# Optimization experiments

Measured on AMD Instinct MI355X. Metric: run time of the kernel, lower is better.

Reference implementation:

```python
import jax, jax.numpy as jnp
import numpy as np

B, N = 4096, 8
C_IMG = 1024          # 256 fpn channels * 4 layers
NODE_CH = 2048        # 8 node concepts * 256
EDGE_CH = 3           # len(edge_concepts) - 1 (HigherPri handled separately)
ACT_CH = 4            # number of unary action predicates
E = N * (N - 1)       # 56 directed edges, fully connected minus self-loops
BBOX_MAX = 1024.0

_idx = np.array([[i, j] for i in range(N) for j in range(N) if i != j], dtype=np.int32)
SRC = jnp.asarray(_idx[:, 0])  # edge_idxs row 0 (message source in PyG NNConv)
DST = jnp.asarray(_idx[:, 1])  # edge_idxs row 1 (aggregation target)


def _lin(key, fin, fout):
    kw, kb = jax.random.split(key)
    s = 1.0 / np.sqrt(fin)
    return (jax.random.uniform(kw, (fin, fout), jnp.float32, -s, s),
            jax.random.uniform(kb, (fout,), jnp.float32, -s, s))


def setup_inputs() -> dict:
    key = jax.random.key(0)
    ks = jax.random.split(key, 16)
    inp = {
        'roi_features': jax.random.normal(ks[0], (B, N, C_IMG), jnp.float32),
        'batch_bboxes': jax.random.uniform(ks[1], (B, N, 4), jnp.float32) * BBOX_MAX,
        'batch_directions': jax.random.normal(ks[2], (B, N, 4), jnp.float32),
        'batch_priorities': jax.random.uniform(ks[3], (B, N), jnp.float32),
    }
    inp['ncp_w1'], inp['ncp_b1'] = _lin(ks[4], C_IMG, 512)
    inp['ncp_w2'], inp['ncp_b2'] = _lin(ks[5], 512, 256)
    inp['ncp_w3'], inp['ncp_b3'] = _lin(ks[6], 256, NODE_CH)
    inp['ep_w1'], inp['ep_b1'] = _lin(ks[7], 8, 256)
    inp['ep_w2'], inp['ep_b2'] = _lin(ks[8], 256, 64)
    inp['ep_w3'], inp['ep_b3'] = _lin(ks[9], 64, (N - 1) * EDGE_CH)
    inp['pr_w1'], inp['pr_b1'] = _lin(ks[10], EDGE_CH + 1, 128)
    inp['pr_w2'], inp['pr_b2'] = _lin(ks[11], 128, NODE_CH * ACT_CH)
    s = 1.0 / np.sqrt(NODE_CH)
    inp['root'] = jax.random.uniform(ks[12], (NODE_CH, ACT_CH), jnp.float32, -s, s)
    inp['bias'] = jnp.zeros((ACT_CH,), jnp.float32)
    return inp


def reference(roi_features, batch_bboxes, batch_directions, batch_priorities,
              ncp_w1, ncp_b1, ncp_w2, ncp_b2, ncp_w3, ncp_b3,
              ep_w1, ep_b1, ep_w2, ep_b2, ep_w3, ep_b3,
              pr_w1, pr_b1, pr_w2, pr_b2, root, bias):
    # node concept predictor: 3-layer MLP + sigmoid over [B, N, C_IMG]
    h = jax.nn.relu(roi_features @ ncp_w1 + ncp_b1)
    h = jax.nn.relu(h @ ncp_w2 + ncp_b2)
    node_concepts = jax.nn.sigmoid(h @ ncp_w3 + ncp_b3)           # [B, N, NODE_CH]

    # edge predictor from bbox (normalized) + direction attributes
    node_attr = jnp.concatenate([batch_bboxes / BBOX_MAX, batch_directions], axis=-1)  # [B,N,8]
    g = jax.nn.relu(node_attr @ ep_w1 + ep_b1)
    g = jax.nn.relu(g @ ep_w2 + ep_b2)
    edge_attr = jax.nn.sigmoid(g @ ep_w3 + ep_b3).reshape(B, N * (N - 1), EDGE_CH)

    # HigherPri channel; original slices pri_mask[:, :, :N-1] (slice [:, :, N:] is empty)
    pri_mask = (batch_priorities[:, :, None] > batch_priorities[:, None, :]).astype(jnp.float32)
    higher_pri = pri_mask[:, :, :N - 1].reshape(B, -1)            # [B, E]
    edge_attr = jnp.concatenate([edge_attr, higher_pri[..., None]], axis=-1)  # [B,E,4]

    # NNConv on batch element 0 only (as in the original forward)
    x = node_concepts[0]                                          # [N, NODE_CH]
    e = edge_attr[0]                                              # [E, EDGE_CH+1]
    w = jax.nn.relu(e @ pr_w1 + pr_b1) @ pr_w2 + pr_b2            # [E, NODE_CH*ACT_CH]
    w = w.reshape(E, NODE_CH, ACT_CH)
    msg = jnp.einsum('ec,eco->eo', x[SRC], w)                     # [E, ACT_CH]
    agg = jax.ops.segment_sum(msg, DST, num_segments=N)           # [N, ACT_CH]
    return agg + x @ root + bias
```

## Files before the change

kernel.cpp:

```cpp
#include <hip/hip_runtime.h>
#include <math.h>

#define CIMG  1024
#define H1F   512
#define H2F   256
#define NODE  2048

#define OFF_H1P  0
#define OFF_H2P  65536
#define OFF_XP   98304
#define OFF_Y2P  163840
#define OFF_EW   172032

__global__ __launch_bounds__(256) void k1_l1_edge(
    const float* __restrict__ roi, const float* __restrict__ w1,
    const float* __restrict__ bbox, const float* __restrict__ dir,
    const float* __restrict__ pri,
    const float* __restrict__ ew1, const float* __restrict__ eb1,
    const float* __restrict__ ew2, const float* __restrict__ eb2,
    const float* __restrict__ ew3, const float* __restrict__ eb3,
    const float* __restrict__ pw1, const float* __restrict__ pb1,
    float* __restrict__ h1part, float* __restrict__ ew_out)
{
    __shared__ float smem[2912];
    const int tid = threadIdx.x;
    const int b = blockIdx.x;

    if (b < 32) {
        float* xin = smem;
        const int kbeg = (b >> 1) * 64;
        const int cbase = (b & 1) * 256;
        for (int idx = tid; idx < 512; idx += 256) {
            int r = idx >> 6, kk = idx & 63;
            xin[idx] = roi[r * CIMG + kbeg + kk];
        }
        __syncthreads();
        const int c = cbase + tid;
        float acc[8] = {0, 0, 0, 0, 0, 0, 0, 0};
        const float* Wp = w1 + (size_t)kbeg * H1F + c;
#pragma unroll 4
        for (int kk = 0; kk < 64; ++kk) {
            float w = Wp[(size_t)kk * H1F];
#pragma unroll
            for (int r = 0; r < 8; ++r) acc[r] += xin[r * 64 + kk] * w;
        }
        float* outp = h1part + (b >> 1) * 4096;
#pragma unroll
        for (int r = 0; r < 8; ++r) outp[r * H1F + c] = acc[r];
        return;
    }

    float* attr = smem;
    float* g1   = smem + 64;
    float* g2   = smem + 2112;
    float* ebuf = smem + 2624;

    if (tid < 64) {
        int r = tid >> 3, j = tid & 7;
        attr[r * 8 + j] = (j < 4) ? bbox[r * 4 + j] * (1.0f / 1024.0f)
                                  : dir[r * 4 + (j - 4)];
    }
    __syncthreads();

    {
        int cc = tid;
        for (int r = 0; r < 8; ++r) {
            float s = eb1[cc];
#pragma unroll
            for (int j = 0; j < 8; ++j) s += attr[r * 8 + j] * ew1[j * 256 + cc];
            g1[r * 256 + cc] = s > 0.f ? s : 0.f;
        }
    }
    __syncthreads();

    for (int idx = tid; idx < 512; idx += 256) {
        int r = idx >> 6, cc = idx & 63;
        float s = eb2[cc];
        for (int j = 0; j < 256; ++j) s += g1[r * 256 + j] * ew2[j * 64 + cc];
        g2[idx] = s > 0.f ? s : 0.f;
    }
    __syncthreads();

    if (tid < 168) {
        int r = tid / 21, q = tid % 21;
        float s = eb3[q];
        for (int j = 0; j < 64; ++j) s += g2[r * 64 + j] * ew3[j * 21 + q];
        ebuf[(tid / 3) * 4 + (tid % 3)] = 1.f / (1.f + expf(-s));
    }
    if (tid < 56) {
        ebuf[tid * 4 + 3] = (pri[tid / 7] > pri[tid % 7]) ? 1.f : 0.f;
    }
    __syncthreads();

    for (int idx = tid; idx < 56 * 128; idx += 256) {
        int e = idx >> 7, t = idx & 127;
        float s = pb1[t];
#pragma unroll
        for (int ch = 0; ch < 4; ++ch) s += ebuf[e * 4 + ch] * pw1[ch * 128 + t];
        ew_out[idx] = s > 0.f ? s : 0.f;
    }
}

__global__ __launch_bounds__(256) void k2_l2(
    const float* __restrict__ h1part, const float* __restrict__ b1,
    const float* __restrict__ w2, float* __restrict__ h2part)
{
    __shared__ float xin[8 * 32];
    const int tid = threadIdx.x;
    const int kbeg = blockIdx.x * 32;

    if (tid < 256) {
        int r = tid >> 5, kk = tid & 31;
        int k = kbeg + kk;
        float v = b1[k];
#pragma unroll
        for (int p = 0; p < 16; ++p) v += h1part[p * 4096 + r * H1F + k];
        xin[r * 32 + kk] = v > 0.f ? v : 0.f;
    }
    __syncthreads();

    const int c = tid;
    float acc[8] = {0, 0, 0, 0, 0, 0, 0, 0};
    const float* Wp = w2 + (size_t)kbeg * H2F + c;
#pragma unroll 4
    for (int kk = 0; kk < 32; ++kk) {
        float w = Wp[(size_t)kk * H2F];
#pragma unroll
        for (int r = 0; r < 8; ++r) acc[r] += xin[r * 32 + kk] * w;
    }
    float* outp = h2part + blockIdx.x * 2048;
#pragma unroll
    for (int r = 0; r < 8; ++r) outp[r * H2F + c] = acc[r];
}

__global__ __launch_bounds__(256) void k3_l3(
    const float* __restrict__ h2part, const float* __restrict__ b2,
    const float* __restrict__ w3, float* __restrict__ xpart)
{
    __shared__ float xin[8 * 64];
    const int tid = threadIdx.x;
    const int kc = blockIdx.x >> 3;
    const int cbase = (blockIdx.x & 7) * 256;
    const int kbeg = kc * 64;

    for (int idx = tid; idx < 512; idx += 256) {
        int r = idx >> 6, kk = idx & 63;
        int k = kbeg + kk;
        float v = b2[k];
#pragma unroll
        for (int p = 0; p < 16; ++p) v += h2part[p * 2048 + r * H2F + k];
        xin[idx] = v > 0.f ? v : 0.f;
    }
    __syncthreads();

    const int c = cbase + tid;
    float acc[8] = {0, 0, 0, 0, 0, 0, 0, 0};
    const float* Wp = w3 + (size_t)kbeg * NODE + c;
#pragma unroll 4
    for (int kk = 0; kk < 64; ++kk) {
        float w = Wp[(size_t)kk * NODE];
#pragma unroll
        for (int r = 0; r < 8; ++r) acc[r] += xin[r * 64 + kk] * w;
    }
    float* outp = xpart + kc * 16384;
#pragma unroll
    for (int r = 0; r < 8; ++r) outp[r * NODE + c] = acc[r];
}

__global__ __launch_bounds__(256) void k4_y2(
    const float* __restrict__ xpart, const float* __restrict__ b3,
    const float* __restrict__ pw2, float* __restrict__ y2part)
{
    const int t = blockIdx.x;
    const int half = blockIdx.y;
    __shared__ float shx[8 * 1024];
    __shared__ float redbuf[4 * 32];
    const int tid = threadIdx.x;

    for (int i = tid; i < 8192; i += 256) {
        int r = i >> 10, cl = i & 1023;
        int c = half * 1024 + cl;
        float v = b3[c];
#pragma unroll
        for (int p = 0; p < 4; ++p) v += xpart[p * 16384 + r * NODE + c];
        shx[i] = 1.f / (1.f + expf(-v));
    }
    __syncthreads();

    float part[8] = {0, 0, 0, 0, 0, 0, 0, 0};
    const float* row = pw2 + (size_t)t * 8192 + half * 4096;
#pragma unroll 4
    for (int it = 0; it < 16; ++it) {
        int j = tid + it * 256;
        float w = row[j];
        int cl = j >> 2;
#pragma unroll
        for (int s = 0; s < 8; ++s) part[s] += shx[s * 1024 + cl] * w;
    }

    const int lane = tid & 63, wave = tid >> 6;
#pragma unroll
    for (int s = 0; s < 8; ++s) {
        part[s] += __shfl_xor(part[s], 4);
        part[s] += __shfl_xor(part[s], 8);
        part[s] += __shfl_xor(part[s], 16);
        part[s] += __shfl_xor(part[s], 32);
    }
    if (lane < 4) {
#pragma unroll
        for (int s = 0; s < 8; ++s) redbuf[wave * 32 + s * 4 + lane] = part[s];
    }
    __syncthreads();
    if (tid < 32) {
        float v = redbuf[tid] + redbuf[32 + tid] + redbuf[64 + tid] + redbuf[96 + tid];
        int s = tid >> 2, o = tid & 3;
        y2part[half * 4096 + (s * 128 + t) * 4 + o] = v;
    }
}

__global__ __launch_bounds__(1024) void k5_final(
    const float* __restrict__ xpart, const float* __restrict__ b3,
    const float* __restrict__ pb2, const float* __restrict__ root,
    const float* __restrict__ bias, const float* __restrict__ ew,
    const float* __restrict__ y2part, float* __restrict__ out)
{
    __shared__ float sdotb[8][2][4], sxr[8][2][4], sagg[8][4];
    const int tid = threadIdx.x;
    const int lane = tid & 63, wave = tid >> 6;

    if (tid < 32) sagg[tid >> 2][tid & 3] = 0.f;
    __syncthreads();

    {
        const int s = wave >> 1, half = wave & 1;
        float pd[4] = {0, 0, 0, 0}, pr[4] = {0, 0, 0, 0};
#pragma unroll 4
        for (int k = 0; k < 16; ++k) {
            int c = half * 1024 + k * 64 + lane;
            float v = b3[c];
#pragma unroll
            for (int p = 0; p < 4; ++p) v += xpart[p * 16384 + s * NODE + c];
            float xv = 1.f / (1.f + expf(-v));
            float4 bv = ((const float4*)pb2)[c];
            float4 rv = ((const float4*)root)[c];
            pd[0] += xv * bv.x; pd[1] += xv * bv.y;
            pd[2] += xv * bv.z; pd[3] += xv * bv.w;
            pr[0] += xv * rv.x; pr[1] += xv * rv.y;
            pr[2] += xv * rv.z; pr[3] += xv * rv.w;
        }
#pragma unroll
        for (int o = 0; o < 4; ++o) {
            for (int off = 32; off; off >>= 1) {
                pd[o] += __shfl_xor(pd[o], off);
                pr[o] += __shfl_xor(pr[o], off);
            }
        }
        if (lane == 0) {
#pragma unroll
            for (int o = 0; o < 4; ++o) {
                sdotb[s][half][o] = pd[o];
                sxr[s][half][o] = pr[o];
            }
        }
    }

    const float* y2a = y2part;
    const float* y2b = y2part + 4096;
    for (int e = wave; e < 56; e += 16) {
        int i = e / 7, jj = e % 7;
        int dst = jj + (jj >= i ? 1 : 0);
        int src = i;
        float pm[4] = {0, 0, 0, 0};
#pragma unroll
        for (int half = 0; half < 2; ++half) {
            int t = lane + half * 64;
            float w = ew[e * 128 + t];
            float4 ya = ((const float4*)y2a)[src * 128 + t];
            float4 yb = ((const float4*)y2b)[src * 128 + t];
            pm[0] += w * (ya.x + yb.x); pm[1] += w * (ya.y + yb.y);
            pm[2] += w * (ya.z + yb.z); pm[3] += w * (ya.w + yb.w);
        }
#pragma unroll
        for (int o = 0; o < 4; ++o)
            for (int off = 32; off; off >>= 1) pm[o] += __shfl_xor(pm[o], off);
        if (lane == 0) {
#pragma unroll
            for (int o = 0; o < 4; ++o) atomicAdd(&sagg[dst][o], pm[o]);
        }
    }
    __syncthreads();

    if (tid < 32) {
        int n = tid >> 2, o = tid & 3;
        float totd = 0.f;
#pragma unroll
        for (int s = 0; s < 8; ++s) totd += sdotb[s][0][o] + sdotb[s][1][o];
        float dn = sdotb[n][0][o] + sdotb[n][1][o];
        float xr = sxr[n][0][o] + sxr[n][1][o];
        out[tid] = sagg[n][o] + (totd - dn) + xr + bias[o];
    }
}

extern "C" void kernel_launch(void* const* d_in, const int* in_sizes, int n_in,
                              void* d_out, int out_size, void* d_ws, size_t ws_size,
                              hipStream_t stream)
{
    (void)in_sizes; (void)n_in; (void)out_size; (void)ws_size;

    const float* roi    = (const float*)d_in[0];
    const float* bbox   = (const float*)d_in[1];
    const float* dirs   = (const float*)d_in[2];
    const float* pri    = (const float*)d_in[3];
    const float* ncp_w1 = (const float*)d_in[4];
    const float* ncp_b1 = (const float*)d_in[5];
    const float* ncp_w2 = (const float*)d_in[6];
    const float* ncp_b2 = (const float*)d_in[7];
    const float* ncp_w3 = (const float*)d_in[8];
    const float* ncp_b3 = (const float*)d_in[9];
    const float* ep_w1  = (const float*)d_in[10];
    const float* ep_b1  = (const float*)d_in[11];
    const float* ep_w2  = (const float*)d_in[12];
    const float* ep_b2  = (const float*)d_in[13];
    const float* ep_w3  = (const float*)d_in[14];
    const float* ep_b3  = (const float*)d_in[15];
    const float* pr_w1  = (const float*)d_in[16];
    const float* pr_b1  = (const float*)d_in[17];
    const float* pr_w2  = (const float*)d_in[18];
    const float* pr_b2  = (const float*)d_in[19];
    const float* root   = (const float*)d_in[20];
    const float* bias   = (const float*)d_in[21];

    float* ws     = (float*)d_ws;
    float* h1part = ws + OFF_H1P;
    float* h2part = ws + OFF_H2P;
    float* xpart  = ws + OFF_XP;
    float* y2part = ws + OFF_Y2P;
    float* ewbuf  = ws + OFF_EW;

    dim3 blk(256);
    k1_l1_edge<<<33, blk, 0, stream>>>(roi, ncp_w1, bbox, dirs, pri,
                                       ep_w1, ep_b1, ep_w2, ep_b2, ep_w3, ep_b3,
                                       pr_w1, pr_b1, h1part, ewbuf);
    k2_l2<<<16, blk, 0, stream>>>(h1part, ncp_b1, ncp_w2, h2part);
    k3_l3<<<32, blk, 0, stream>>>(h2part, ncp_b2, ncp_w3, xpart);
    k4_y2<<<dim3(128, 2), blk, 0, stream>>>(xpart, ncp_b3, pr_w2, y2part);
    k5_final<<<1, dim3(1024), 0, stream>>>(xpart, ncp_b3, pr_b2, root, bias,
                                           ewbuf, y2part, (float*)d_out);
}
```

Baseline: 262.5 us.

## Fuse all five stages into one cooperative kernel with grid syncs

Replaces the five separate kernel launches with a single cooperative kernel of 256 blocks that separates the stages with grid-wide barriers. Layer 1 is split across 64 blocks with a smaller K chunk, and the x·bias and x·root dot products move into the y2 stage, with results passed through a workspace buffer. The final aggregation then runs in one 256-thread block. The aim is to remove per-launch overhead and gaps between kernels, at the cost of grid-sync latency and fewer waves in the final step.

```diff
diff --git a/kernel.cpp b/kernel.cpp
--- a/kernel.cpp
+++ b/kernel.cpp
@@ -1,5 +1,8 @@
 #include <hip/hip_runtime.h>
+#include <hip/hip_cooperative_groups.h>
 #include <math.h>
+
+namespace cg = cooperative_groups;
 
 #define CIMG  1024
 #define H1F   512
@@ -7,297 +10,279 @@
 #define NODE  2048
 
 #define OFF_H1P  0
-#define OFF_H2P  65536
-#define OFF_XP   98304
-#define OFF_Y2P  163840
-#define OFF_EW   172032
-
-__global__ __launch_bounds__(256) void k1_l1_edge(
-    const float* __restrict__ roi, const float* __restrict__ w1,
-    const float* __restrict__ bbox, const float* __restrict__ dir,
+#define OFF_H2P  131072
+#define OFF_XP   163840
+#define OFF_Y2P  229376
+#define OFF_EW   237568
+#define OFF_DX   244736
+
+__global__ __launch_bounds__(256) void coop_all(
+    const float* __restrict__ roi,
+    const float* __restrict__ bbox, const float* __restrict__ dirs,
     const float* __restrict__ pri,
-    const float* __restrict__ ew1, const float* __restrict__ eb1,
-    const float* __restrict__ ew2, const float* __restrict__ eb2,
-    const float* __restrict__ ew3, const float* __restrict__ eb3,
-    const float* __restrict__ pw1, const float* __restrict__ pb1,
-    float* __restrict__ h1part, float* __restrict__ ew_out)
+    const float* __restrict__ ncp_w1, const float* __restrict__ ncp_b1,
+    const float* __restrict__ ncp_w2, const float* __restrict__ ncp_b2,
+    const float* __restrict__ ncp_w3, const float* __restrict__ ncp_b3,
+    const float* __restrict__ ep_w1, const float* __restrict__ ep_b1,
+    const float* __restrict__ ep_w2, const float* __restrict__ ep_b2,
+    const float* __restrict__ ep_w3, const float* __restrict__ ep_b3,
+    const float* __restrict__ pr_w1, const float* __restrict__ pr_b1,
+    const float* __restrict__ pr_w2, const float* __restrict__ pr_b2,
+    const float* __restrict__ root, const float* __restrict__ bias,
+    float* __restrict__ h1part, float* __restrict__ h2part,
+    float* __restrict__ xpart, float* __restrict__ y2part,
+    float* __restrict__ ewbuf, float* __restrict__ dotxr,
+    float* __restrict__ out)
 {
-    __shared__ float smem[2912];
+    cg::grid_group grid = cg::this_grid();
+    __shared__ float smem[8320];
+    const int b = blockIdx.x;
     const int tid = threadIdx.x;
-    const int b = blockIdx.x;
+    const int lane = tid & 63, wave = tid >> 6;
+
+    if (b < 64) {
+        const int kc = b >> 1;
+        const int kbeg = kc * 32;
+        const int cbase = (b & 1) * 256;
+        {
+            int r = tid >> 5, kk = tid & 31;
+            smem[tid] = roi[r * CIMG + kbeg + kk];
+        }
+        __syncthreads();
+        const int c = cbase + tid;
+        float acc[8] = {0, 0, 0, 0, 0, 0, 0, 0};
+        const float* Wp = ncp_w1 + (size_t)kbeg * H1F + c;
+#pragma unroll 8
+        for (int kk = 0; kk < 32; ++kk) {
+            float w = Wp[(size_t)kk * H1F];
+#pragma unroll
+            for (int r = 0; r < 8; ++r) acc[r] += smem[r * 32 + kk] * w;
+        }
+        float* outp = h1part + kc * 4096;
+#pragma unroll
+        for (int r = 0; r < 8; ++r) outp[r * H1F + c] = acc[r];
+    } else if (b == 64) {
+        float* attr = smem;
+        float* g1   = smem + 64;
+        float* g2   = smem + 2112;
+        float* ebuf = smem + 2624;
+        if (tid < 64) {
+            int r = tid >> 3, j = tid & 7;
+            attr[r * 8 + j] = (j < 4) ? bbox[r * 4 + j] * (1.0f / 1024.0f)
+                                      : dirs[r * 4 + (j - 4)];
+        }
+        __syncthreads();
+        {
+            int cc = tid;
+            for (int r = 0; r < 8; ++r) {
+                float s = ep_b1[cc];
+#pragma unroll
+                for (int j = 0; j < 8; ++j) s += attr[r * 8 + j] * ep_w1[j * 256 + cc];
+                g1[r * 256 + cc] = s > 0.f ? s : 0.f;
+            }
+        }
+        __syncthreads();
+        for (int idx = tid; idx < 512; idx += 256) {
+            int r = idx >> 6, cc = idx & 63;
+            float s = ep_b2[cc];
+            for (int j = 0; j < 256; ++j) s += g1[r * 256 + j] * ep_w2[j * 64 + cc];
+            g2[idx] = s > 0.f ? s : 0.f;
+        }
+        __syncthreads();
+        if (tid < 168) {
+            int r = tid / 21, q = tid % 21;
+            float s = ep_b3[q];
+            for (int j = 0; j < 64; ++j) s += g2[r * 64 + j] * ep_w3[j * 21 + q];
+            ebuf[(tid / 3) * 4 + (tid % 3)] = 1.f / (1.f + expf(-s));
+        }
+        if (tid < 56) {
+            ebuf[tid * 4 + 3] = (pri[tid / 7] > pri[tid % 7]) ? 1.f : 0.f;
+        }
+        __syncthreads();
+        for (int idx = tid; idx < 56 * 128; idx += 256) {
+            int e = idx >> 7, t = idx & 127;
+            float s = pr_b1[t];
+#pragma unroll
+            for (int ch = 0; ch < 4; ++ch) s += ebuf[e * 4 + ch] * pr_w1[ch * 128 + t];
+            ewbuf[idx] = s > 0.f ? s : 0.f;
+        }
+    }
+    grid.sync();
+
+    if (b < 16) {
+        const int kbeg = b * 32;
+        {
+            int r = tid >> 5, kk = tid & 31;
+            int k = kbeg + kk;
+            float v = ncp_b1[k];
+#pragma unroll
+            for (int p = 0; p < 32; ++p) v += h1part[p * 4096 + r * H1F + k];
+            smem[tid] = v > 0.f ? v : 0.f;
+        }
+        __syncthreads();
+        const int c = tid;
+        float acc[8] = {0, 0, 0, 0, 0, 0, 0, 0};
+        const float* Wp = ncp_w2 + (size_t)kbeg * H2F + c;
+#pragma unroll 8
+        for (int kk = 0; kk < 32; ++kk) {
+            float w = Wp[(size_t)kk * H2F];
+#pragma unroll
+            for (int r = 0; r < 8; ++r) acc[r] += smem[r * 32 + kk] * w;
+        }
+        float* outp = h2part + b * 2048;
+#pragma unroll
+        for (int r = 0; r < 8; ++r) outp[r * H2F + c] = acc[r];
+    }
+    grid.sync();
 
     if (b < 32) {
-        float* xin = smem;
-        const int kbeg = (b >> 1) * 64;
-        const int cbase = (b & 1) * 256;
+        const int kc = b >> 3;
+        const int cbase = (b & 7) * 256;
+        const int kbeg = kc * 64;
         for (int idx = tid; idx < 512; idx += 256) {
             int r = idx >> 6, kk = idx & 63;
-            xin[idx] = roi[r * CIMG + kbeg + kk];
+            int k = kbeg + kk;
+            float v = ncp_b2[k];
+#pragma unroll
+            for (int p = 0; p < 16; ++p) v += h2part[p * 2048 + r * H2F + k];
+            smem[idx] = v > 0.f ? v : 0.f;
         }
         __syncthreads();
         const int c = cbase + tid;
         float acc[8] = {0, 0, 0, 0, 0, 0, 0, 0};
-        const float* Wp = w1 + (size_t)kbeg * H1F + c;
+        const float* Wp = ncp_w3 + (size_t)kbeg * NODE + c;
 #pragma unroll 4
         for (int kk = 0; kk < 64; ++kk) {
-            float w = Wp[(size_t)kk * H1F];
-#pragma unroll
-            for (int r = 0; r < 8; ++r) acc[r] += xin[r * 64 + kk] * w;
-        }
-        float* outp = h1part + (b >> 1) * 4096;
-#pragma unroll
-        for (int r = 0; r < 8; ++r) outp[r * H1F + c] = acc[r];
-        return;
-    }
-
-    float* attr = smem;
-    float* g1   = smem + 64;
-    float* g2   = smem + 2112;
-    float* ebuf = smem + 2624;
-
-    if (tid < 64) {
-        int r = tid >> 3, j = tid & 7;
-        attr[r * 8 + j] = (j < 4) ? bbox[r * 4 + j] * (1.0f / 1024.0f)
-                                  : dir[r * 4 + (j - 4)];
-    }
-    __syncthreads();
+            float w = Wp[(size_t)kk * NODE];
+#pragma unroll
+            for (int r = 0; r < 8; ++r) acc[r] += smem[r * 64 + kk] * w;
+        }
+        float* outp = xpart + kc * 16384;
+#pragma unroll
+        for (int r = 0; r < 8; ++r) outp[r * NODE + c] = acc[r];
+    }
+    grid.sync();
 
     {
-        int cc = tid;
-        for (int r = 0; r < 8; ++r) {
-            float s = eb1[cc];
-#pragma unroll
-            for (int j = 0; j < 8; ++j) s += attr[r * 8 + j] * ew1[j * 256 + cc];
-            g1[r * 256 + cc] = s > 0.f ? s : 0.f;
-        }
-    }
-    __syncthreads();
-
-    for (int idx = tid; idx < 512; idx += 256) {
-        int r = idx >> 6, cc = idx & 63;
-        float s = eb2[cc];
-        for (int j = 0; j < 256; ++j) s += g1[r * 256 + j] * ew2[j * 64 + cc];
-        g2[idx] = s > 0.f ? s : 0.f;
-    }
-    __syncthreads();
-
-    if (tid < 168) {
-        int r = tid / 21, q = tid % 21;
-        float s = eb3[q];
-        for (int j = 0; j < 64; ++j) s += g2[r * 64 + j] * ew3[j * 21 + q];
-        ebuf[(tid / 3) * 4 + (tid % 3)] = 1.f / (1.f + expf(-s));
-    }
-    if (tid < 56) {
-        ebuf[tid * 4 + 3] = (pri[tid / 7] > pri[tid % 7]) ? 1.f : 0.f;
-    }
-    __syncthreads();
-
-    for (int idx = tid; idx < 56 * 128; idx += 256) {
-        int e = idx >> 7, t = idx & 127;
-        float s = pb1[t];
-#pragma unroll
-        for (int ch = 0; ch < 4; ++ch) s += ebuf[e * 4 + ch] * pw1[ch * 128 + t];
-        ew_out[idx] = s > 0.f ? s : 0.f;
-    }
-}
-
-__global__ __launch_bounds__(256) void k2_l2(
-    const float* __restrict__ h1part, const float* __restrict__ b1,
-    const float* __restrict__ w2, float* __restrict__ h2part)
-{
-    __shared__ float xin[8 * 32];
-    const int tid = threadIdx.x;
-    const int kbeg = blockIdx.x * 32;
-
-    if (tid < 256) {
-        int r = tid >> 5, kk = tid & 31;
-        int k = kbeg + kk;
-        float v = b1[k];
-#pragma unroll
-        for (int p = 0; p < 16; ++p) v += h1part[p * 4096 + r * H1F + k];
-        xin[r * 32 + kk] = v > 0.f ? v : 0.f;
-    }
-    __syncthreads();
-
-    const int c = tid;
-    float acc[8] = {0, 0, 0, 0, 0, 0, 0, 0};
-    const float* Wp = w2 + (size_t)kbeg * H2F + c;
+        const int t = b >> 1;
+        const int half = b & 1;
+        float* shx = smem;
+        float* redbuf = smem + 8192;
+        for (int i = tid; i < 8192; i += 256) {
+            int r = i >> 10, cl = i & 1023;
+            int c = half * 1024 + cl;
+            float v = ncp_b3[c];
+#pragma unroll
+            for (int p = 0; p < 4; ++p) v += xpart[p * 16384 + r * NODE + c];
+            shx[i] = 1.f / (1.f + expf(-v));
+        }
+        __syncthreads();
+
+        float part[8] = {0, 0, 0, 0, 0, 0, 0, 0};
+        const float* row = pr_w2 + (size_t)t * 8192 + half * 4096;
 #pragma unroll 4
-    for (int kk = 0; kk < 32; ++kk) {
-        float w = Wp[(size_t)kk * H2F];
-#pragma unroll
-        for (int r = 0; r < 8; ++r) acc[r] += xin[r * 32 + kk] * w;
-    }
-    float* outp = h2part + blockIdx.x * 2048;
-#pragma unroll
-    for (int r = 0; r < 8; ++r) outp[r * H2F + c] = acc[r];
-}
-
-__global__ __launch_bounds__(256) void k3_l3(
-    const float* __restrict__ h2part, const float* __restrict__ b2,
-    const float* __restrict__ w3, float* __restrict__ xpart)
-{
-    __shared__ float xin[8 * 64];
-    const int tid = threadIdx.x;
-    const int kc = blockIdx.x >> 3;
-    const int cbase = (blockIdx.x & 7) * 256;
-    const int kbeg = kc * 64;
-
-    for (int idx = tid; idx < 512; idx += 256) {
-        int r = idx >> 6, kk = idx & 63;
-        int k = kbeg + kk;
-        float v = b2[k];
-#pragma unroll
-        for (int p = 0; p < 16; ++p) v += h2part[p * 2048 + r * H2F + k];
-        xin[idx] = v > 0.f ? v : 0.f;
-    }
-    __syncthreads();
-
-    const int c = cbase + tid;
-    float acc[8] = {0, 0, 0, 0, 0, 0, 0, 0};
-    const float* Wp = w3 + (size_t)kbeg * NODE + c;
+        for (int it = 0; it < 16; ++it) {
+            int j = tid + it * 256;
+            float w = row[j];
+            int cl = j >> 2;
+#pragma unroll
+            for (int s = 0; s < 8; ++s) part[s] += shx[s * 1024 + cl] * w;
+        }
+#pragma unroll
+        for (int s = 0; s < 8; ++s) {
+            part[s] += __shfl_xor(part[s], 4);
+            part[s] += __shfl_xor(part[s], 8);
+            part[s] += __shfl_xor(part[s], 16);
+            part[s] += __shfl_xor(part[s], 32);
+        }
+        if (lane < 4) {
+#pragma unroll
+            for (int s = 0; s < 8; ++s) redbuf[wave * 32 + s * 4 + lane] = part[s];
+        }
+        __syncthreads();
+        if (tid < 32) {
+            float v = redbuf[tid] + redbuf[32 + tid] + redbuf[64 + tid] + redbuf[96 + tid];
+            int s = tid >> 2, o = tid & 3;
+            y2part[half * 4096 + (s * 128 + t) * 4 + o] = v;
+        }
+
+        if (t == 0) {
+#pragma unroll
+            for (int si = 0; si < 2; ++si) {
+                const int s = wave * 2 + si;
+                float pd[4] = {0, 0, 0, 0}, pr[4] = {0, 0, 0, 0};
 #pragma unroll 4
-    for (int kk = 0; kk < 64; ++kk) {
-        float w = Wp[(size_t)kk * NODE];
-#pragma unroll
-        for (int r = 0; r < 8; ++r) acc[r] += xin[r * 64 + kk] * w;
-    }
-    float* outp = xpart + kc * 16384;
-#pragma unroll
-    for (int r = 0; r < 8; ++r) outp[r * NODE + c] = acc[r];
-}
-
-__global__ __launch_bounds__(256) void k4_y2(
-    const float* __restrict__ xpart, const float* __restrict__ b3,
-    const float* __restrict__ pw2, float* __restrict__ y2part)
-{
-    const int t = blockIdx.x;
-    const int half = blockIdx.y;
-    __shared__ float shx[8 * 1024];
-    __shared__ float redbuf[4 * 32];
-    const int tid = threadIdx.x;
-
-    for (int i = tid; i < 8192; i += 256) {
-        int r = i >> 10, cl = i & 1023;
-        int c = half * 1024 + cl;
-        float v = b3[c];
-#pragma unroll
-        for (int p = 0; p < 4; ++p) v += xpart[p * 16384 + r * NODE + c];
-        shx[i] = 1.f / (1.f + expf(-v));
-    }
-    __syncthreads();
-
-    float part[8] = {0, 0, 0, 0, 0, 0, 0, 0};
-    const float* row = pw2 + (size_t)t * 8192 + half * 4096;
-#pragma unroll 4
-    for (int it = 0; it < 16; ++it) {
-        int j = tid + it * 256;
-        float w = row[j];
-        int cl = j >> 2;
-#pragma unroll
-        for (int s = 0; s < 8; ++s) part[s] += shx[s * 1024 + cl] * w;
-    }
-
-    const int lane = tid & 63, wave = tid >> 6;
-#pragma unroll
-    for (int s = 0; s < 8; ++s) {
-        part[s] += __shfl_xor(part[s], 4);
-        part[s] += __shfl_xor(part[s], 8);
-        part[s] += __shfl_xor(part[s], 16);
-        part[s] += __shfl_xor(part[s], 32);
-    }
-    if (lane < 4) {
-#pragma unroll
-        for (int s = 0; s < 8; ++s) redbuf[wave * 32 + s * 4 + lane] = part[s];
-    }
-    __syncthreads();
-    if (tid < 32) {
-        float v = redbuf[tid] + redbuf[32 + tid] + redbuf[64 + tid] + redbuf[96 + tid];
-        int s = tid >> 2, o = tid & 3;
-        y2part[half * 4096 + (s * 128 + t) * 4 + o] = v;
-    }
-}
-
-__global__ __launch_bounds__(1024) void k5_final(
-    const float* __restrict__ xpart, const float* __restrict__ b3,
-    const float* __restrict__ pb2, const float* __restrict__ root,
-    const float* __restrict__ bias, const float* __restrict__ ew,
-    const float* __restrict__ y2part, float* __restrict__ out)
-{
-    __shared__ float sdotb[8][2][4], sxr[8][2][4], sagg[8][4];
-    const int tid = threadIdx.x;
-    const int lane = tid & 63, wave = tid >> 6;
-
-    if (tid < 32) sagg[tid >> 2][tid & 3] = 0.f;
-    __syncthreads();
-
-    {
-        const int s = wave >> 1, half = wave & 1;
-        float pd[4] = {0, 0, 0, 0}, pr[4] = {0, 0, 0, 0};
-#pragma unroll 4
-        for (int k = 0; k < 16; ++k) {
-            int c = half * 1024 + k * 64 + lane;
-            float v = b3[c];
-#pragma unroll
-            for (int p = 0; p < 4; ++p) v += xpart[p * 16384 + s * NODE + c];
-            float xv = 1.f / (1.f + expf(-v));
-            float4 bv = ((const float4*)pb2)[c];
-            float4 rv = ((const float4*)root)[c];
-            pd[0] += xv * bv.x; pd[1] += xv * bv.y;
-            pd[2] += xv * bv.z; pd[3] += xv * bv.w;
-            pr[0] += xv * rv.x; pr[1] += xv * rv.y;
-            pr[2] += xv * rv.z; pr[3] += xv * rv.w;
-        }
-#pragma unroll
-        for (int o = 0; o < 4; ++o) {
-            for (int off = 32; off; off >>= 1) {
-                pd[o] += __shfl_xor(pd[o], off);
-                pr[o] += __shfl_xor(pr[o], off);
+                for (int it = 0; it < 16; ++it) {
+                    int cl = it * 64 + lane;
+                    float xv = shx[s * 1024 + cl];
+                    int c = half * 1024 + cl;
+                    float4 bv = ((const float4*)pr_b2)[c];
+                    float4 rv = ((const float4*)root)[c];
+                    pd[0] += xv * bv.x; pd[1] += xv * bv.y;
+                    pd[2] += xv * bv.z; pd[3] += xv * bv.w;
+                    pr[0] += xv * rv.x; pr[1] += xv * rv.y;
+                    pr[2] += xv * rv.z; pr[3] += xv * rv.w;
+                }
+#pragma unroll
+                for (int o = 0; o < 4; ++o) {
+                    for (int off = 32; off; off >>= 1) {
+                        pd[o] += __shfl_xor(pd[o], off);
+                        pr[o] += __shfl_xor(pr[o], off);
+                    }
+                }
+                if (lane == 0) {
+#pragma unroll
+                    for (int o = 0; o < 4; ++o) {
+                        dotxr[half * 32 + s * 4 + o] = pd[o];
+                        dotxr[64 + half * 32 + s * 4 + o] = pr[o];
+                    }
+                }
             }
         }
-        if (lane == 0) {
-#pragma unroll
-            for (int o = 0; o < 4; ++o) {
-                sdotb[s][half][o] = pd[o];
-                sxr[s][half][o] = pr[o];
+    }
+    grid.sync();
+
+    if (b == 0) {
+        float* sagg = smem;
+        if (tid < 32) sagg[tid] = 0.f;
+        __syncthreads();
+
+        const float* y2a = y2part;
+        const float* y2b = y2part + 4096;
+        for (int e = wave; e < 56; e += 4) {
+            int i = e / 7, jj = e % 7;
+            int dst = jj + (jj >= i ? 1 : 0);
+            int src = i;
+            float pm[4] = {0, 0, 0, 0};
+#pragma unroll
+            for (int half = 0; half < 2; ++half) {
+                int t = lane + half * 64;
+                float w = ewbuf[e * 128 + t];
+                float4 ya = ((const float4*)y2a)[src * 128 + t];
+                float4 yb = ((const float4*)y2b)[src * 128 + t];
+                pm[0] += w * (ya.x + yb.x); pm[1] += w * (ya.y + yb.y);
+                pm[2] += w * (ya.z + yb.z); pm[3] += w * (ya.w + yb.w);
             }
-        }
-    }
-
-    const float* y2a = y2part;
-    const float* y2b = y2part + 4096;
-    for (int e = wave; e < 56; e += 16) {
-        int i = e / 7, jj = e % 7;
-        int dst = jj + (jj >= i ? 1 : 0);
-        int src = i;
-        float pm[4] = {0, 0, 0, 0};
-#pragma unroll
-        for (int half = 0; half < 2; ++half) {
-            int t = lane + half * 64;
-            float w = ew[e * 128 + t];
-            float4 ya = ((const float4*)y2a)[src * 128 + t];
-            float4 yb = ((const float4*)y2b)[src * 128 + t];
-            pm[0] += w * (ya.x + yb.x); pm[1] += w * (ya.y + yb.y);
-            pm[2] += w * (ya.z + yb.z); pm[3] += w * (ya.w + yb.w);
-        }
-#pragma unroll
-        for (int o = 0; o < 4; ++o)
-            for (int off = 32; off; off >>= 1) pm[o] += __shfl_xor(pm[o], off);
-        if (lane == 0) {
-#pragma unroll
-            for (int o = 0; o < 4; ++o) atomicAdd(&sagg[dst][o], pm[o]);
-        }
-    }
-    __syncthreads();
-
-    if (tid < 32) {
-        int n = tid >> 2, o = tid & 3;
-        float totd = 0.f;
-#pragma unroll
-        for (int s = 0; s < 8; ++s) totd += sdotb[s][0][o] + sdotb[s][1][o];
-        float dn = sdotb[n][0][o] + sdotb[n][1][o];
-        float xr = sxr[n][0][o] + sxr[n][1][o];
-        out[tid] = sagg[n][o] + (totd - dn) + xr + bias[o];
+#pragma unroll
+            for (int o = 0; o < 4; ++o)
+                for (int off = 32; off; off >>= 1) pm[o] += __shfl_xor(pm[o], off);
+            if (lane == 0) {
+#pragma unroll
+                for (int o = 0; o < 4; ++o) atomicAdd(&sagg[dst * 4 + o], pm[o]);
+            }
+        }
+        __syncthreads();
+
+        if (tid < 32) {
+            int n = tid >> 2, o = tid & 3;
+            float totd = 0.f;
+#pragma unroll
+            for (int s = 0; s < 8; ++s)
+                totd += dotxr[s * 4 + o] + dotxr[32 + s * 4 + o];
+            float dn = dotxr[n * 4 + o] + dotxr[32 + n * 4 + o];
+            float xr = dotxr[64 + n * 4 + o] + dotxr[96 + n * 4 + o];
+            out[tid] = sagg[tid] + (totd - dn) + xr + bias[o];
+        }
     }
 }
 
@@ -336,14 +321,21 @@
     float* xpart  = ws + OFF_XP;
     float* y2part = ws + OFF_Y2P;
     float* ewbuf  = ws + OFF_EW;
-
-    dim3 blk(256);
-    k1_l1_edge<<<33, blk, 0, stream>>>(roi, ncp_w1, bbox, dirs, pri,
-                                       ep_w1, ep_b1, ep_w2, ep_b2, ep_w3, ep_b3,
-                                       pr_w1, pr_b1, h1part, ewbuf);
-    k2_l2<<<16, blk, 0, stream>>>(h1part, ncp_b1, ncp_w2, h2part);
-    k3_l3<<<32, blk, 0, stream>>>(h2part, ncp_b2, ncp_w3, xpart);
-    k4_y2<<<dim3(128, 2), blk, 0, stream>>>(xpart, ncp_b3, pr_w2, y2part);
-    k5_final<<<1, dim3(1024), 0, stream>>>(xpart, ncp_b3, pr_b2, root, bias,
-                                           ewbuf, y2part, (float*)d_out);
+    float* dotxr  = ws + OFF_DX;
+    float* outp   = (float*)d_out;
+
+    void* args[] = {
+        (void*)&roi, (void*)&bbox, (void*)&dirs, (void*)&pri,
+        (void*)&ncp_w1, (void*)&ncp_b1, (void*)&ncp_w2, (void*)&ncp_b2,
+        (void*)&ncp_w3, (void*)&ncp_b3,
+        (void*)&ep_w1, (void*)&ep_b1, (void*)&ep_w2, (void*)&ep_b2,
+        (void*)&ep_w3, (void*)&ep_b3,
+        (void*)&pr_w1, (void*)&pr_b1, (void*)&pr_w2, (void*)&pr_b2,
+        (void*)&root, (void*)&bias,
+        (void*)&h1part, (void*)&h2part, (void*)&xpart, (void*)&y2part,
+        (void*)&ewbuf, (void*)&dotxr, (void*)&outp
+    };
+
+    hipLaunchCooperativeKernel((void*)coop_all, dim3(256), dim3(256),
+                               args, 0, stream);
 }
```

Result: slower. 387.9 us (+47.8%).

## Fuse MLP layers 2-3 and merge y2 with final aggregation via atomics

Applied to the files above, without the earlier changes.

The five-kernel pipeline becomes three. Layers 2 and 3 of the node MLP are fused into one kernel in which each of 16 blocks redundantly recomputes the full layer-2 activations and then produces a slice of the sigmoid node features. The y2 projection is fused with the edge-weighted aggregation and the root/bias terms, and results are accumulated straight into the output with global atomics, which the first kernel zeroes. This removes two launches and the intermediate partial buffers, at the cost of redundant layer-2 work, 1024-thread blocks and float atomic ordering nondeterminism.

```diff
diff --git a/kernel.cpp b/kernel.cpp
--- a/kernel.cpp
+++ b/kernel.cpp
@@ -7,10 +7,8 @@
 #define NODE  2048
 
 #define OFF_H1P  0
-#define OFF_H2P  65536
-#define OFF_XP   98304
-#define OFF_Y2P  163840
-#define OFF_EW   172032
+#define OFF_X    65536
+#define OFF_EW   81920
 
 __global__ __launch_bounds__(256) void k1_l1_edge(
     const float* __restrict__ roi, const float* __restrict__ w1,
@@ -20,9 +18,10 @@
     const float* __restrict__ ew2, const float* __restrict__ eb2,
     const float* __restrict__ ew3, const float* __restrict__ eb3,
     const float* __restrict__ pw1, const float* __restrict__ pb1,
-    float* __restrict__ h1part, float* __restrict__ ew_out)
+    float* __restrict__ h1part, float* __restrict__ ew_out,
+    float* __restrict__ out)
 {
-    __shared__ float smem[2912];
+    __shared__ float smem[2848];
     const int tid = threadIdx.x;
     const int b = blockIdx.x;
 
@@ -50,6 +49,8 @@
         return;
     }
 
+    if (tid < 32) out[tid] = 0.f;
+
     float* attr = smem;
     float* g1   = smem + 64;
     float* g2   = smem + 2112;
@@ -61,7 +62,6 @@
                                   : dir[r * 4 + (j - 4)];
     }
     __syncthreads();
-
     {
         int cc = tid;
         for (int r = 0; r < 8; ++r) {
@@ -72,7 +72,6 @@
         }
     }
     __syncthreads();
-
     for (int idx = tid; idx < 512; idx += 256) {
         int r = idx >> 6, cc = idx & 63;
         float s = eb2[cc];
@@ -80,7 +79,6 @@
         g2[idx] = s > 0.f ? s : 0.f;
     }
     __syncthreads();
-
     if (tid < 168) {
         int r = tid / 21, q = tid % 21;
         float s = eb3[q];
@@ -91,7 +89,6 @@
         ebuf[tid * 4 + 3] = (pri[tid / 7] > pri[tid % 7]) ? 1.f : 0.f;
     }
     __syncthreads();
-
     for (int idx = tid; idx < 56 * 128; idx += 256) {
         int e = idx >> 7, t = idx & 127;
         float s = pb1[t];
@@ -101,89 +98,81 @@
     }
 }
 
-__global__ __launch_bounds__(256) void k2_l2(
+__global__ __launch_bounds__(1024) void k2_l23(
     const float* __restrict__ h1part, const float* __restrict__ b1,
-    const float* __restrict__ w2, float* __restrict__ h2part)
+    const float* __restrict__ w2, const float* __restrict__ b2,
+    const float* __restrict__ w3, const float* __restrict__ b3,
+    float* __restrict__ x)
 {
-    __shared__ float xin[8 * 32];
+    __shared__ float h1[4096];
+    __shared__ float h2p[8192];
+    __shared__ float h2[2048];
     const int tid = threadIdx.x;
-    const int kbeg = blockIdx.x * 32;
-
-    if (tid < 256) {
-        int r = tid >> 5, kk = tid & 31;
-        int k = kbeg + kk;
+
+    for (int idx = tid; idx < 4096; idx += 1024) {
+        int k = idx & 511;
         float v = b1[k];
 #pragma unroll
-        for (int p = 0; p < 16; ++p) v += h1part[p * 4096 + r * H1F + k];
-        xin[r * 32 + kk] = v > 0.f ? v : 0.f;
-    }
-    __syncthreads();
-
-    const int c = tid;
-    float acc[8] = {0, 0, 0, 0, 0, 0, 0, 0};
-    const float* Wp = w2 + (size_t)kbeg * H2F + c;
-#pragma unroll 4
-    for (int kk = 0; kk < 32; ++kk) {
-        float w = Wp[(size_t)kk * H2F];
-#pragma unroll
-        for (int r = 0; r < 8; ++r) acc[r] += xin[r * 32 + kk] * w;
-    }
-    float* outp = h2part + blockIdx.x * 2048;
-#pragma unroll
-    for (int r = 0; r < 8; ++r) outp[r * H2F + c] = acc[r];
+        for (int p = 0; p < 16; ++p) v += h1part[p * 4096 + idx];
+        h1[idx] = v > 0.f ? v : 0.f;
+    }
+    __syncthreads();
+
+    {
+        const int c = tid & 255, kg = tid >> 8;
+        float acc[8] = {0, 0, 0, 0, 0, 0, 0, 0};
+        const float* Wp = w2 + (size_t)(kg * 128) * H2F + c;
+        const float* h1p = h1 + kg * 128;
+#pragma unroll 4
+        for (int kk = 0; kk < 128; ++kk) {
+            float w = Wp[(size_t)kk * H2F];
+#pragma unroll
+            for (int r = 0; r < 8; ++r) acc[r] += h1p[r * 512 + kk] * w;
+        }
+#pragma unroll
+        for (int r = 0; r < 8; ++r) h2p[kg * 2048 + r * 256 + c] = acc[r];
+    }
+    __syncthreads();
+    for (int idx = tid; idx < 2048; idx += 1024) {
+        int c = idx & 255;
+        float v = b2[c] + h2p[idx] + h2p[2048 + idx] + h2p[4096 + idx] + h2p[6144 + idx];
+        h2[idx] = v > 0.f ? v : 0.f;
+    }
+    __syncthreads();
+
+    {
+        const int c = blockIdx.x * 128 + (tid & 127);
+        const int r = tid >> 7;
+        float acc = b3[c];
+        const float* Wp = w3 + c;
+        const float* h2r = h2 + r * 256;
+#pragma unroll 4
+        for (int k = 0; k < 256; ++k)
+            acc += h2r[k] * Wp[(size_t)k * NODE];
+        x[r * NODE + c] = 1.f / (1.f + expf(-acc));
+    }
 }
 
-__global__ __launch_bounds__(256) void k3_l3(
-    const float* __restrict__ h2part, const float* __restrict__ b2,
-    const float* __restrict__ w3, float* __restrict__ xpart)
+__global__ __launch_bounds__(256) void k3_y2_final(
+    const float* __restrict__ x, const float* __restrict__ pw2,
+    const float* __restrict__ pb2, const float* __restrict__ root,
+    const float* __restrict__ bias, const float* __restrict__ ew,
+    float* __restrict__ out)
 {
-    __shared__ float xin[8 * 64];
+    __shared__ float shx[8192];
+    __shared__ float redbuf[128];
+    __shared__ float ylocal[32];
+    __shared__ float aggl[32];
+    __shared__ float dotl[32], xrl[32];
+    const int t = blockIdx.x >> 1;
+    const int half = blockIdx.x & 1;
     const int tid = threadIdx.x;
-    const int kc = blockIdx.x >> 3;
-    const int cbase = (blockIdx.x & 7) * 256;
-    const int kbeg = kc * 64;
-
-    for (int idx = tid; idx < 512; idx += 256) {
-        int r = idx >> 6, kk = idx & 63;
-        int k = kbeg + kk;
-        float v = b2[k];
-#pragma unroll
-        for (int p = 0; p < 16; ++p) v += h2part[p * 2048 + r * H2F + k];
-        xin[idx] = v > 0.f ? v : 0.f;
-    }
-    __syncthreads();
-
-    const int c = cbase + tid;
-    float acc[8] = {0, 0, 0, 0, 0, 0, 0, 0};
-    const float* Wp = w3 + (size_t)kbeg * NODE + c;
-#pragma unroll 4
-    for (int kk = 0; kk < 64; ++kk) {
-        float w = Wp[(size_t)kk * NODE];
-#pragma unroll
-        for (int r = 0; r < 8; ++r) acc[r] += xin[r * 64 + kk] * w;
-    }
-    float* outp = xpart + kc * 16384;
-#pragma unroll
-    for (int r = 0; r < 8; ++r) outp[r * NODE + c] = acc[r];
-}
-
-__global__ __launch_bounds__(256) void k4_y2(
-    const float* __restrict__ xpart, const float* __restrict__ b3,
-    const float* __restrict__ pw2, float* __restrict__ y2part)
-{
-    const int t = blockIdx.x;
-    const int half = blockIdx.y;
-    __shared__ float shx[8 * 1024];
-    __shared__ float redbuf[4 * 32];
-    const int tid = threadIdx.x;
-
+    const int lane = tid & 63, wave = tid >> 6;
+
+    if (tid < 32) aggl[tid] = 0.f;
     for (int i = tid; i < 8192; i += 256) {
         int r = i >> 10, cl = i & 1023;
-        int c = half * 1024 + cl;
-        float v = b3[c];
-#pragma unroll
-        for (int p = 0; p < 4; ++p) v += xpart[p * 16384 + r * NODE + c];
-        shx[i] = 1.f / (1.f + expf(-v));
+        shx[i] = x[r * NODE + half * 1024 + cl];
     }
     __syncthreads();
 
@@ -197,8 +186,6 @@
 #pragma unroll
         for (int s = 0; s < 8; ++s) part[s] += shx[s * 1024 + cl] * w;
     }
-
-    const int lane = tid & 63, wave = tid >> 6;
 #pragma unroll
     for (int s = 0; s < 8; ++s) {
         part[s] += __shfl_xor(part[s], 4);
@@ -211,93 +198,62 @@
         for (int s = 0; s < 8; ++s) redbuf[wave * 32 + s * 4 + lane] = part[s];
     }
     __syncthreads();
-    if (tid < 32) {
-        float v = redbuf[tid] + redbuf[32 + tid] + redbuf[64 + tid] + redbuf[96 + tid];
-        int s = tid >> 2, o = tid & 3;
-        y2part[half * 4096 + (s * 128 + t) * 4 + o] = v;
-    }
-}
-
-__global__ __launch_bounds__(1024) void k5_final(
-    const float* __restrict__ xpart, const float* __restrict__ b3,
-    const float* __restrict__ pb2, const float* __restrict__ root,
-    const float* __restrict__ bias, const float* __restrict__ ew,
-    const float* __restrict__ y2part, float* __restrict__ out)
-{
-    __shared__ float sdotb[8][2][4], sxr[8][2][4], sagg[8][4];
-    const int tid = threadIdx.x;
-    const int lane = tid & 63, wave = tid >> 6;
-
-    if (tid < 32) sagg[tid >> 2][tid & 3] = 0.f;
-    __syncthreads();
-
-    {
-        const int s = wave >> 1, half = wave & 1;
-        float pd[4] = {0, 0, 0, 0}, pr[4] = {0, 0, 0, 0};
-#pragma unroll 4
-        for (int k = 0; k < 16; ++k) {
-            int c = half * 1024 + k * 64 + lane;
-            float v = b3[c];
-#pragma unroll
-            for (int p = 0; p < 4; ++p) v += xpart[p * 16384 + s * NODE + c];
-            float xv = 1.f / (1.f + expf(-v));
-            float4 bv = ((const float4*)pb2)[c];
-            float4 rv = ((const float4*)root)[c];
-            pd[0] += xv * bv.x; pd[1] += xv * bv.y;
-            pd[2] += xv * bv.z; pd[3] += xv * bv.w;
-            pr[0] += xv * rv.x; pr[1] += xv * rv.y;
-            pr[2] += xv * rv.z; pr[3] += xv * rv.w;
-        }
-#pragma unroll
-        for (int o = 0; o < 4; ++o) {
-            for (int off = 32; off; off >>= 1) {
-                pd[o] += __shfl_xor(pd[o], off);
-                pr[o] += __shfl_xor(pr[o], off);
-            }
-        }
-        if (lane == 0) {
-#pragma unroll
-            for (int o = 0; o < 4; ++o) {
-                sdotb[s][half][o] = pd[o];
-                sxr[s][half][o] = pr[o];
-            }
-        }
-    }
-
-    const float* y2a = y2part;
-    const float* y2b = y2part + 4096;
-    for (int e = wave; e < 56; e += 16) {
+    if (tid < 32)
+        ylocal[tid] = redbuf[tid] + redbuf[32 + tid] + redbuf[64 + tid] + redbuf[96 + tid];
+    __syncthreads();
+
+    if (tid < 224) {
+        int e = tid >> 2, o = tid & 3;
         int i = e / 7, jj = e % 7;
         int dst = jj + (jj >= i ? 1 : 0);
-        int src = i;
-        float pm[4] = {0, 0, 0, 0};
-#pragma unroll
-        for (int half = 0; half < 2; ++half) {
-            int t = lane + half * 64;
-            float w = ew[e * 128 + t];
-            float4 ya = ((const float4*)y2a)[src * 128 + t];
-            float4 yb = ((const float4*)y2b)[src * 128 + t];
-            pm[0] += w * (ya.x + yb.x); pm[1] += w * (ya.y + yb.y);
-            pm[2] += w * (ya.z + yb.z); pm[3] += w * (ya.w + yb.w);
-        }
-#pragma unroll
-        for (int o = 0; o < 4; ++o)
-            for (int off = 32; off; off >>= 1) pm[o] += __shfl_xor(pm[o], off);
-        if (lane == 0) {
-#pragma unroll
-            for (int o = 0; o < 4; ++o) atomicAdd(&sagg[dst][o], pm[o]);
-        }
-    }
-    __syncthreads();
-
-    if (tid < 32) {
-        int n = tid >> 2, o = tid & 3;
-        float totd = 0.f;
-#pragma unroll
-        for (int s = 0; s < 8; ++s) totd += sdotb[s][0][o] + sdotb[s][1][o];
-        float dn = sdotb[n][0][o] + sdotb[n][1][o];
-        float xr = sxr[n][0][o] + sxr[n][1][o];
-        out[tid] = sagg[n][o] + (totd - dn) + xr + bias[o];
+        float v = ew[e * 128 + t] * ylocal[i * 4 + o];
+        atomicAdd(&aggl[dst * 4 + o], v);
+    }
+    __syncthreads();
+    if (tid < 32) atomicAdd(&out[tid], aggl[tid]);
+
+    if (t == 0) {
+#pragma unroll
+        for (int si = 0; si < 2; ++si) {
+            const int s = wave * 2 + si;
+            float pd[4] = {0, 0, 0, 0}, pr[4] = {0, 0, 0, 0};
+#pragma unroll 4
+            for (int it = 0; it < 16; ++it) {
+                int cl = it * 64 + lane;
+                float xv = shx[s * 1024 + cl];
+                int c = half * 1024 + cl;
+                float4 bv = ((const float4*)pb2)[c];
+                float4 rv = ((const float4*)root)[c];
+                pd[0] += xv * bv.x; pd[1] += xv * bv.y;
+                pd[2] += xv * bv.z; pd[3] += xv * bv.w;
+                pr[0] += xv * rv.x; pr[1] += xv * rv.y;
+                pr[2] += xv * rv.z; pr[3] += xv * rv.w;
+            }
+#pragma unroll
+            for (int o = 0; o < 4; ++o) {
+                for (int off = 32; off; off >>= 1) {
+                    pd[o] += __shfl_xor(pd[o], off);
+                    pr[o] += __shfl_xor(pr[o], off);
+                }
+            }
+            if (lane == 0) {
+#pragma unroll
+                for (int o = 0; o < 4; ++o) {
+                    dotl[s * 4 + o] = pd[o];
+                    xrl[s * 4 + o] = pr[o];
+                }
+            }
+        }
+        __syncthreads();
+        if (tid < 32) {
+            int n = tid >> 2, o = tid & 3;
+            float totd = 0.f;
+#pragma unroll
+            for (int s = 0; s < 8; ++s) totd += dotl[s * 4 + o];
+            float v = (totd - dotl[n * 4 + o]) + xrl[n * 4 + o]
+                    + (half == 0 ? bias[o] : 0.f);
+            atomicAdd(&out[tid], v);
+        }
     }
 }
 
@@ -332,18 +288,16 @@
 
     float* ws     = (float*)d_ws;
     float* h1part = ws + OFF_H1P;
-    float* h2part = ws + OFF_H2P;
-    float* xpart  = ws + OFF_XP;
-    float* y2part = ws + OFF_Y2P;
+    float* x      = ws + OFF_X;
     float* ewbuf  = ws + OFF_EW;
-
-    dim3 blk(256);
-    k1_l1_edge<<<33, blk, 0, stream>>>(roi, ncp_w1, bbox, dirs, pri,
-                                       ep_w1, ep_b1, ep_w2, ep_b2, ep_w3, ep_b3,
-                                       pr_w1, pr_b1, h1part, ewbuf);
-    k2_l2<<<16, blk, 0, stream>>>(h1part, ncp_b1, ncp_w2, h2part);
-    k3_l3<<<32, blk, 0, stream>>>(h2part, ncp_b2, ncp_w3, xpart);
-    k4_y2<<<dim3(128, 2), blk, 0, stream>>>(xpart, ncp_b3, pr_w2, y2part);
-    k5_final<<<1, dim3(1024), 0, stream>>>(xpart, ncp_b3, pr_b2, root, bias,
-                                           ewbuf, y2part, (float*)d_out);
+    float* outp   = (float*)d_out;
+
+    k1_l1_edge<<<33, dim3(256), 0, stream>>>(roi, ncp_w1, bbox, dirs, pri,
+                                             ep_w1, ep_b1, ep_w2, ep_b2,
+                                             ep_w3, ep_b3, pr_w1, pr_b1,
+                                             h1part, ewbuf, outp);
+    k2_l23<<<16, dim3(1024), 0, stream>>>(h1part, ncp_b1, ncp_w2, ncp_b2,
+                                          ncp_w3, ncp_b3, x);
+    k3_y2_final<<<256, dim3(256), 0, stream>>>(x, pr_w2, pr_b2, root, bias,
+                                               ewbuf, outp);
 }
```

Measured after the change: 276.3 us. 1.05x slower.
